# Kernel optimization log

Measured on AMD Instinct MI355X. Metric: run time of the kernel, lower is better.

The kernel has to match this reference:

```python
import jax, jax.numpy as jnp
import numpy as np

# ChebConv normalization (sym, lambda_max=2.0 default):
# L_hat = 2/lambda_max * (I - D^-1/2 A D^-1/2) - I = -D^-1/2 A D^-1/2 (plus 0/-1 diag for deg>0/deg==0)

def _norm(edge_weight, src, dst, N):
    deg = jax.ops.segment_sum(edge_weight, src, num_segments=N)
    d = jnp.where(deg > 0, deg ** -0.5, 0.0)
    norm = -d[src] * edge_weight * d[dst]          # off-diagonal entries of L_hat
    diag = d * d * deg - 1.0                        # 0 where deg>0, -1 where deg==0
    return norm, diag

def _prop(z, norm, diag, src, dst, N):
    # y = L_hat @ z, message passing source->target
    agg = jax.ops.segment_sum(norm[:, None] * z[src], dst, num_segments=N)
    return agg + diag[:, None] * z

def _cheb(h, theta, bias, norm, diag, src, dst, N):
    # theta: [K, H, H]; Chebyshev recurrence T_k = 2 L_hat T_{k-1} - T_{k-2}
    Tx0 = h
    out = Tx0 @ theta[0]
    Tx1 = _prop(Tx0, norm, diag, src, dst, N)
    out = out + Tx1 @ theta[1]
    for k in range(2, theta.shape[0]):
        Tx2 = 2.0 * _prop(Tx1, norm, diag, src, dst, N) - Tx0
        out = out + Tx2 @ theta[k]
        Tx0, Tx1 = Tx1, Tx2
    return out + bias

def setup_inputs() -> dict:
    N, E, F_IN, H, K = 50000, 1600000, 64, 64, 3
    key = jax.random.key(0)
    ks = jax.random.split(key, 12)
    s = 0.05
    x = jax.random.normal(ks[0], (N, F_IN), jnp.float32)
    edge_index = jax.random.randint(ks[1], (2, E), 0, N, jnp.int32)
    edge_weight = jax.random.uniform(ks[2], (E,), jnp.float32)
    h = jax.random.normal(ks[3], (N, H), jnp.float32)
    c = jax.random.normal(ks[4], (N, H), jnp.float32)
    W_x = jax.random.normal(ks[5], (4, F_IN, H), jnp.float32) * s   # W_i, W_f, W_c, W_o
    w_c = jax.random.normal(ks[6], (3, H), jnp.float32) * s          # w_c_i, w_c_f, w_c_o
    b = jax.random.normal(ks[7], (4, H), jnp.float32) * s            # b_i, b_f, b_c, b_o
    theta = jax.random.normal(ks[8], (4, K, H, H), jnp.float32) * s  # ChebConv weights per gate
    conv_b = jax.random.normal(ks[9], (4, H), jnp.float32) * s       # ChebConv biases per gate
    lin_w = jax.random.normal(ks[10], (H, H), jnp.float32) * s
    lin_b = jax.random.normal(ks[11], (H,), jnp.float32) * s
    return dict(x=x, edge_index=edge_index, edge_weight=edge_weight, h=h, c=c,
                W_x=W_x, w_c=w_c, b=b, theta=theta, conv_b=conv_b,
                lin_w=lin_w, lin_b=lin_b)

def reference(x, edge_index, edge_weight, h, c, W_x, w_c, b, theta, conv_b, lin_w, lin_b):
    N = x.shape[0]
    src, dst = edge_index[0], edge_index[1]
    norm, diag = _norm(edge_weight, src, dst, N)
    I = jax.nn.sigmoid(x @ W_x[0] + _cheb(h, theta[0], conv_b[0], norm, diag, src, dst, N) + w_c[0] * c + b[0])
    Fg = jax.nn.sigmoid(x @ W_x[1] + _cheb(h, theta[1], conv_b[1], norm, diag, src, dst, N) + w_c[1] * c + b[1])
    T = jnp.tanh(x @ W_x[2] + _cheb(h, theta[2], conv_b[2], norm, diag, src, dst, N) + b[2])
    Cn = Fg * c + I * T
    O = jax.nn.sigmoid(x @ W_x[3] + _cheb(h, theta[3], conv_b[3], norm, diag, src, dst, N) + w_c[2] * Cn + b[3])
    Hn = O * jnp.tanh(Cn)
    h_out = jax.nn.relu(Hn) @ lin_w + lin_b
    return (h_out, Hn, Cn)
```

## Files before the change

### kernel.cpp

```cpp
#include <hip/hip_runtime.h>
#include <math.h>


#define KCAP 80

__global__ void init_pack(float* __restrict__ deg, int* __restrict__ cnt,
                          const float* __restrict__ W_x, const float* __restrict__ theta,
                          float* __restrict__ Wbig, int N) {
    int idx = blockIdx.x * blockDim.x + threadIdx.x;
    if (idx < N) { deg[idx] = 0.f; cnt[idx] = 0; }
    if (idx < 4 * 64 * 256) {
        int s = idx >> 14;
        int rem = idx & 16383;
        int k = rem >> 8;
        int cj = rem & 255;
        int g = cj >> 6;
        int j = cj & 63;
        float v = (s == 0) ? W_x[((size_t)g * 64 + k) * 64 + j]
                           : theta[(((size_t)g * 3 + (s - 1)) * 64 + k) * 64 + j];
        Wbig[idx] = v;
    }
}

__global__ void edge_fused(const int* __restrict__ ei, const float* __restrict__ w,
                           float* __restrict__ deg, int* __restrict__ cnt,
                           int2* __restrict__ slots, int E) {
    int t = blockIdx.x * blockDim.x + threadIdx.x;
    int e = t * 4;
    if (e + 3 < E && (E & 3) == 0) {
        int4 s4 = *reinterpret_cast<const int4*>(ei + e);
        int4 d4 = *reinterpret_cast<const int4*>(ei + E + e);
        float4 w4 = *reinterpret_cast<const float4*>(w + e);
        atomicAdd(&deg[s4.x], w4.x);
        atomicAdd(&deg[s4.y], w4.y);
        atomicAdd(&deg[s4.z], w4.z);
        atomicAdd(&deg[s4.w], w4.w);
        int p0 = atomicAdd(&cnt[d4.x], 1);
        int p1 = atomicAdd(&cnt[d4.y], 1);
        int p2 = atomicAdd(&cnt[d4.z], 1);
        int p3 = atomicAdd(&cnt[d4.w], 1);
        if (p0 < KCAP) slots[(size_t)d4.x * KCAP + p0] = make_int2(s4.x, __float_as_int(w4.x));
        if (p1 < KCAP) slots[(size_t)d4.y * KCAP + p1] = make_int2(s4.y, __float_as_int(w4.y));
        if (p2 < KCAP) slots[(size_t)d4.z * KCAP + p2] = make_int2(s4.z, __float_as_int(w4.z));
        if (p3 < KCAP) slots[(size_t)d4.w * KCAP + p3] = make_int2(s4.w, __float_as_int(w4.w));
    } else {
        for (int q = e; q < e + 4 && q < E; ++q) {
            int s = ei[q];
            int d = ei[E + q];
            float wv = w[q];
            atomicAdd(&deg[s], wv);
            int p = atomicAdd(&cnt[d], 1);
            if (p < KCAP) slots[(size_t)d * KCAP + p] = make_int2(s, __float_as_int(wv));
        }
    }
}

__global__ __launch_bounds__(256)
void node_prep(const float* __restrict__ deg, const float* __restrict__ h,
               float* __restrict__ dinv, float* __restrict__ diagv,
               float* __restrict__ zs1, int N) {
    int idx = blockIdx.x * 256 + threadIdx.x;
    if (idx >= N * 64) return;
    int i = idx >> 6;
    float dg = deg[i];
    float dv = (dg > 0.f) ? 1.0f / sqrtf(dg) : 0.f;
    if ((idx & 63) == 0) {
        dinv[i] = dv;
        diagv[i] = (dg > 0.f) ? dv * dv * dg - 1.0f : -1.0f;
    }
    zs1[idx] = dv * h[idx];
}

__global__ __launch_bounds__(256)
void spmm_slots(const float* __restrict__ zfull, const float* __restrict__ zsc,
                const float* __restrict__ diagv, const float* __restrict__ dinv,
                const int* __restrict__ cnt, const int2* __restrict__ slots,
                const float* __restrict__ hsub, float alpha,
                float* __restrict__ out, float* __restrict__ zscOut, int N) {
    const int wq = __builtin_amdgcn_readfirstlane(threadIdx.x >> 6);
    const int r = blockIdx.x * 4 + wq;
    const int lane = threadIdx.x & 63;
    if (r >= N) return;
    const int n = min(cnt[r], KCAP);
    const float dgv = diagv[r];
    const float dvv = dinv[r];
    float g = 0.f;
    const int4* s4 = reinterpret_cast<const int4*>(slots + (size_t)r * KCAP);
    int p = 0;
    for (; p + 7 < n; p += 8) {
        const int q = p >> 1;
        int4 a = s4[q + 0];
        int4 b = s4[q + 1];
        int4 cc = s4[q + 2];
        int4 d = s4[q + 3];
        float z0 = zsc[(size_t)a.x * 64 + lane];
        float z1 = zsc[(size_t)a.z * 64 + lane];
        float z2 = zsc[(size_t)b.x * 64 + lane];
        float z3 = zsc[(size_t)b.z * 64 + lane];
        float z4 = zsc[(size_t)cc.x * 64 + lane];
        float z5 = zsc[(size_t)cc.z * 64 + lane];
        float z6 = zsc[(size_t)d.x * 64 + lane];
        float z7 = zsc[(size_t)d.z * 64 + lane];
        g += __int_as_float(a.y) * z0;
        g += __int_as_float(a.w) * z1;
        g += __int_as_float(b.y) * z2;
        g += __int_as_float(b.w) * z3;
        g += __int_as_float(cc.y) * z4;
        g += __int_as_float(cc.w) * z5;
        g += __int_as_float(d.y) * z6;
        g += __int_as_float(d.w) * z7;
    }
    const int2* s2 = slots + (size_t)r * KCAP;
    for (; p < n; ++p) {
        int2 eSlot = s2[p];
        g += __int_as_float(eSlot.y) * zsc[(size_t)eSlot.x * 64 + lane];
    }
    float val = dgv * zfull[(size_t)r * 64 + lane] - dvv * g;
    float res = alpha * val;
    if (hsub) res -= hsub[(size_t)r * 64 + lane];
    out[(size_t)r * 64 + lane] = res;
    if (zscOut) zscOut[(size_t)r * 64 + lane] = dvv * res;
}

__device__ __forceinline__ float sigf_(float v) { return 1.0f / (1.0f + __expf(-v)); }
__device__ __forceinline__ float tanhf_(float v) { return 2.0f / (1.0f + __expf(-2.0f * v)) - 1.0f; }

__global__ __launch_bounds__(256, 4)
void gemm_gates(const float* __restrict__ x, const float* __restrict__ h,
                const float* __restrict__ Tx1, const float* __restrict__ Tx2,
                const float* __restrict__ Wbig, const float* __restrict__ c,
                const float* __restrict__ w_c, const float* __restrict__ bb,
                const float* __restrict__ conv_b, const float* __restrict__ lin_w,
                const float* __restrict__ lin_b,
                float* __restrict__ out, int N) {
    __shared__ __align__(16) float At[32][64];
    __shared__ __align__(16) float Bs[8192];
    const int tid = threadIdx.x;
    const int tx = tid & 31;
    const int ty = tid >> 5;
    const int row0 = blockIdx.x * 64;

    float acc[8][8];
#pragma unroll
    for (int i = 0; i < 8; ++i)
#pragma unroll
        for (int j = 0; j < 8; ++j) acc[i][j] = 0.f;

    const float* Asrc[4] = {x, h, Tx1, Tx2};

    for (int s = 0; s < 4; ++s) {
        const float* A = Asrc[s];
#pragma unroll
        for (int hf = 0; hf < 2; ++hf) {
            __syncthreads();
            {
                const int mi = tid & 63;
                const int kc = tid >> 6;
                const int gr = row0 + mi;
#pragma unroll
                for (int rep = 0; rep < 2; ++rep) {
                    const int kl = rep * 16 + kc * 4;
                    float4 v = make_float4(0.f, 0.f, 0.f, 0.f);
                    if (gr < N) v = *reinterpret_cast<const float4*>(A + (size_t)gr * 64 + hf * 32 + kl);
                    At[kl + 0][mi] = v.x;
                    At[kl + 1][mi] = v.y;
                    At[kl + 2][mi] = v.z;
                    At[kl + 3][mi] = v.w;
                }
            }
            {
                const float4* B4 = reinterpret_cast<const float4*>(Wbig + ((size_t)s * 64 + hf * 32) * 256);
                float4* Bf4 = reinterpret_cast<float4*>(Bs);
#pragma unroll
                for (int rep = 0; rep < 8; ++rep) {
                    int i4 = rep * 256 + tid;
                    Bf4[i4] = B4[i4];
                }
            }
            __syncthreads();
#pragma unroll 4
            for (int k = 0; k < 32; ++k) {
                float av[8], bv[8];
                *reinterpret_cast<float4*>(av)     = *reinterpret_cast<const float4*>(&At[k][ty * 8]);
                *reinterpret_cast<float4*>(av + 4) = *reinterpret_cast<const float4*>(&At[k][ty * 8 + 4]);
                *reinterpret_cast<float4*>(bv)     = *reinterpret_cast<const float4*>(&Bs[k * 256 + tx * 4]);
                *reinterpret_cast<float4*>(bv + 4) = *reinterpret_cast<const float4*>(&Bs[k * 256 + 128 + tx * 4]);
#pragma unroll
                for (int i = 0; i < 8; ++i)
#pragma unroll
                    for (int j = 0; j < 8; ++j) acc[i][j] += av[i] * bv[j];
            }
        }
    }

    __syncthreads();

    const int jbase = (tx & 15) * 4;
    const bool loT = (tx < 16);
    const size_t No64 = (size_t)N * 64;

    const float4 cbI = *reinterpret_cast<const float4*>(conv_b + jbase);
    const float4 cbF = *reinterpret_cast<const float4*>(conv_b + 64 + jbase);
    const float4 cbT = *reinterpret_cast<const float4*>(conv_b + 128 + jbase);
    const float4 cbO = *reinterpret_cast<const float4*>(conv_b + 192 + jbase);
    const float4 bI  = *reinterpret_cast<const float4*>(bb + jbase);
    const float4 bF  = *reinterpret_cast<const float4*>(bb + 64 + jbase);
    const float4 bT  = *reinterpret_cast<const float4*>(bb + 128 + jbase);
    const float4 bO  = *reinterpret_cast<const float4*>(bb + 192 + jbase);
    const float4 wI  = *reinterpret_cast<const float4*>(w_c + jbase);
    const float4 wF  = *reinterpret_cast<const float4*>(w_c + 64 + jbase);
    const float4 wO  = *reinterpret_cast<const float4*>(w_c + 128 + jbase);

#pragma unroll
    for (int i = 0; i < 8; ++i) {
        const int li = ty * 8 + i;
        const int gi = row0 + li;
        float4 cv4 = make_float4(0.f, 0.f, 0.f, 0.f);
        if (gi < N) cv4 = *reinterpret_cast<const float4*>(c + (size_t)gi * 64 + jbase);
        float hn[4], cn[4];
#pragma unroll
        for (int jj = 0; jj < 4; ++jj) {
            float mine0 = acc[i][jj];
            float mine1 = acc[i][4 + jj];
            float oth0 = __shfl_xor(mine0, 16, 64);
            float oth1 = __shfl_xor(mine1, 16, 64);
            float pI = loT ? mine0 : oth0;
            float pF = loT ? oth0 : mine0;
            float pT = loT ? mine1 : oth1;
            float pO = loT ? oth1 : mine1;
            const float cv = (&cv4.x)[jj];
            pI += (&cbI.x)[jj] + (&bI.x)[jj] + (&wI.x)[jj] * cv;
            pF += (&cbF.x)[jj] + (&bF.x)[jj] + (&wF.x)[jj] * cv;
            pT += (&cbT.x)[jj] + (&bT.x)[jj];
            float Ig = sigf_(pI);
            float Fg = sigf_(pF);
            float Tg = tanhf_(pT);
            float Cn = Fg * cv + Ig * Tg;
            pO += (&cbO.x)[jj] + (&bO.x)[jj] + (&wO.x)[jj] * Cn;
            float Og = sigf_(pO);
            float Hn = Og * tanhf_(Cn);
            hn[jj] = Hn;
            cn[jj] = Cn;
            if (loT) {
                int j = jbase + jj;
                Bs[j * 64 + (((li & ~3) ^ (j & 28)) + (li & 3))] = fmaxf(Hn, 0.f);
            }
        }
        if (gi < N) {
            if (loT)
                *reinterpret_cast<float4*>(out + No64 + (size_t)gi * 64 + jbase) =
                    make_float4(hn[0], hn[1], hn[2], hn[3]);
            else
                *reinterpret_cast<float4*>(out + No64 * 2 + (size_t)gi * 64 + jbase) =
                    make_float4(cn[0], cn[1], cn[2], cn[3]);
        }
    }
    __syncthreads();

    {
        const int ri = tid >> 4;
        const int ci = tid & 15;
        float a2[4][4];
#pragma unroll
        for (int i = 0; i < 4; ++i)
#pragma unroll
            for (int j = 0; j < 4; ++j) a2[i][j] = 0.f;
#pragma unroll 4
        for (int k = 0; k < 64; ++k) {
            float4 av4 = *reinterpret_cast<const float4*>(&Bs[k * 64 + ((ri * 4) ^ (k & 28))]);
            float4 bv4 = *reinterpret_cast<const float4*>(lin_w + k * 64 + ci * 4);
            a2[0][0] += av4.x * bv4.x; a2[0][1] += av4.x * bv4.y; a2[0][2] += av4.x * bv4.z; a2[0][3] += av4.x * bv4.w;
            a2[1][0] += av4.y * bv4.x; a2[1][1] += av4.y * bv4.y; a2[1][2] += av4.y * bv4.z; a2[1][3] += av4.y * bv4.w;
            a2[2][0] += av4.z * bv4.x; a2[2][1] += av4.z * bv4.y; a2[2][2] += av4.z * bv4.z; a2[2][3] += av4.z * bv4.w;
            a2[3][0] += av4.w * bv4.x; a2[3][1] += av4.w * bv4.y; a2[3][2] += av4.w * bv4.z; a2[3][3] += av4.w * bv4.w;
        }
        float4 bias = *reinterpret_cast<const float4*>(lin_b + ci * 4);
#pragma unroll
        for (int i = 0; i < 4; ++i) {
            int gr = row0 + ri * 4 + i;
            if (gr < N) {
                float4 o = make_float4(a2[i][0] + bias.x, a2[i][1] + bias.y,
                                       a2[i][2] + bias.z, a2[i][3] + bias.w);
                *reinterpret_cast<float4*>(out + (size_t)gr * 64 + ci * 4) = o;
            }
        }
    }
}

extern "C" void kernel_launch(void* const* d_in, const int* in_sizes, int n_in,
                              void* d_out, int out_size, void* d_ws, size_t ws_size,
                              hipStream_t stream) {
    const float* x        = (const float*)d_in[0];
    const int* edge_index = (const int*)d_in[1];
    const float* edge_w   = (const float*)d_in[2];
    const float* h        = (const float*)d_in[3];
    const float* c        = (const float*)d_in[4];
    const float* W_x      = (const float*)d_in[5];
    const float* w_c      = (const float*)d_in[6];
    const float* b        = (const float*)d_in[7];
    const float* theta    = (const float*)d_in[8];
    const float* conv_b   = (const float*)d_in[9];
    const float* lin_w    = (const float*)d_in[10];
    const float* lin_b    = (const float*)d_in[11];
    float* out = (float*)d_out;

    const int N = in_sizes[0] / 64;
    const int E = in_sizes[2];

    char* wsb = (char*)d_ws;
    size_t off = 0;
    auto carve = [&](size_t bytes) -> void* {
        void* p = wsb + off;
        off = (off + bytes + 255) & ~(size_t)255;
        return p;
    };
    float* deg   = (float*)carve((size_t)N * 4);
    int*   cnt   = (int*)  carve((size_t)N * 4);
    float* dinv  = (float*)carve((size_t)N * 4);
    float* diagv = (float*)carve((size_t)N * 4);
    int2*  slots = (int2*) carve((size_t)N * KCAP * 8);
    float* Tx1   = (float*)carve((size_t)N * 64 * 4);
    float* Tx2   = (float*)carve((size_t)N * 64 * 4);
    float* zsT   = (float*)carve((size_t)N * 64 * 4);
    float* Wbig  = (float*)carve((size_t)4 * 64 * 256 * 4);
    float* zs1   = Tx2;

    const int initElems = (N > 65536) ? N : 65536;
    init_pack<<<(initElems + 255) / 256, 256, 0, stream>>>(deg, cnt, W_x, theta, Wbig, N);
    edge_fused<<<((E + 3) / 4 + 255) / 256, 256, 0, stream>>>(edge_index, edge_w, deg, cnt, slots, E);
    node_prep<<<((N * 64) + 255) / 256, 256, 0, stream>>>(deg, h, dinv, diagv, zs1, N);
    spmm_slots<<<(N + 3) / 4, 256, 0, stream>>>(h, zs1, diagv, dinv, cnt, slots,
                                                nullptr, 1.0f, Tx1, zsT, N);
    spmm_slots<<<(N + 3) / 4, 256, 0, stream>>>(Tx1, zsT, diagv, dinv, cnt, slots,
                                                h, 2.0f, Tx2, nullptr, N);
    gemm_gates<<<(N + 63) / 64, 256, 0, stream>>>(x, h, Tx1, Tx2, Wbig, c, w_c, b, conv_b,
                                                  lin_w, lin_b, out, N);
}
```

Measured before the change: 525.5 us.

## Overlap x/h gate GEMM with edge scatter and drop pre-scaled z buffers

Fuses the edge atomic scatter with the x and h slices of the gate GEMM into one launch whose blocks interleave, so the compute-bound GEMM hides latency behind the atomic-bound edge pass. The partial products go to a new N×256 PRE buffer that the final gate kernel loads as its starting accumulator, so it only multiplies Tx1 and Tx2. It also removes the pre-scaled zs buffers: node_prep only computes dinv and diag, and the SpMM multiplies by dinv[src] per neighbor. This costs an extra scalar gather per edge and extra PRE read/write traffic, and it depends on the workspace being large enough.

```diff
diff --git a/kernel.cpp b/kernel.cpp
--- a/kernel.cpp
+++ b/kernel.cpp
@@ -22,61 +22,138 @@
     }
 }
 
-__global__ void edge_fused(const int* __restrict__ ei, const float* __restrict__ w,
-                           float* __restrict__ deg, int* __restrict__ cnt,
-                           int2* __restrict__ slots, int E) {
-    int t = blockIdx.x * blockDim.x + threadIdx.x;
-    int e = t * 4;
-    if (e + 3 < E && (E & 3) == 0) {
-        int4 s4 = *reinterpret_cast<const int4*>(ei + e);
-        int4 d4 = *reinterpret_cast<const int4*>(ei + E + e);
-        float4 w4 = *reinterpret_cast<const float4*>(w + e);
-        atomicAdd(&deg[s4.x], w4.x);
-        atomicAdd(&deg[s4.y], w4.y);
-        atomicAdd(&deg[s4.z], w4.z);
-        atomicAdd(&deg[s4.w], w4.w);
-        int p0 = atomicAdd(&cnt[d4.x], 1);
-        int p1 = atomicAdd(&cnt[d4.y], 1);
-        int p2 = atomicAdd(&cnt[d4.z], 1);
-        int p3 = atomicAdd(&cnt[d4.w], 1);
-        if (p0 < KCAP) slots[(size_t)d4.x * KCAP + p0] = make_int2(s4.x, __float_as_int(w4.x));
-        if (p1 < KCAP) slots[(size_t)d4.y * KCAP + p1] = make_int2(s4.y, __float_as_int(w4.y));
-        if (p2 < KCAP) slots[(size_t)d4.z * KCAP + p2] = make_int2(s4.z, __float_as_int(w4.z));
-        if (p3 < KCAP) slots[(size_t)d4.w * KCAP + p3] = make_int2(s4.w, __float_as_int(w4.w));
-    } else {
-        for (int q = e; q < e + 4 && q < E; ++q) {
-            int s = ei[q];
-            int d = ei[E + q];
-            float wv = w[q];
-            atomicAdd(&deg[s], wv);
-            int p = atomicAdd(&cnt[d], 1);
-            if (p < KCAP) slots[(size_t)d * KCAP + p] = make_int2(s, __float_as_int(wv));
+__global__ __launch_bounds__(256, 4)
+void edge_gemmxh(const int* __restrict__ ei, const float* __restrict__ w,
+                 float* __restrict__ deg, int* __restrict__ cnt,
+                 int2* __restrict__ slots, int E, int EB,
+                 const float* __restrict__ x, const float* __restrict__ h,
+                 const float* __restrict__ Wbig, float* __restrict__ PRE,
+                 int N, int GB) {
+    __shared__ __align__(16) float At[32][64];
+    __shared__ __align__(16) float Bs[8192];
+    const int bi = blockIdx.x;
+    bool isGemm;
+    int sub;
+    if (GB > 0 && bi < 2 * GB) { isGemm = (bi & 1); sub = bi >> 1; }
+    else { isGemm = false; sub = GB + (bi - 2 * GB); }
+
+    if (!isGemm) {
+        if (sub >= EB) return;
+        const int e = (sub * 256 + threadIdx.x) * 4;
+        if (e + 3 < E && (E & 3) == 0) {
+            int4 s4 = *reinterpret_cast<const int4*>(ei + e);
+            int4 d4 = *reinterpret_cast<const int4*>(ei + E + e);
+            float4 w4 = *reinterpret_cast<const float4*>(w + e);
+            atomicAdd(&deg[s4.x], w4.x);
+            atomicAdd(&deg[s4.y], w4.y);
+            atomicAdd(&deg[s4.z], w4.z);
+            atomicAdd(&deg[s4.w], w4.w);
+            int p0 = atomicAdd(&cnt[d4.x], 1);
+            int p1 = atomicAdd(&cnt[d4.y], 1);
+            int p2 = atomicAdd(&cnt[d4.z], 1);
+            int p3 = atomicAdd(&cnt[d4.w], 1);
+            if (p0 < KCAP) slots[(size_t)d4.x * KCAP + p0] = make_int2(s4.x, __float_as_int(w4.x));
+            if (p1 < KCAP) slots[(size_t)d4.y * KCAP + p1] = make_int2(s4.y, __float_as_int(w4.y));
+            if (p2 < KCAP) slots[(size_t)d4.z * KCAP + p2] = make_int2(s4.z, __float_as_int(w4.z));
+            if (p3 < KCAP) slots[(size_t)d4.w * KCAP + p3] = make_int2(s4.w, __float_as_int(w4.w));
+        } else {
+            for (int q = e; q < e + 4 && q < E; ++q) {
+                int s = ei[q];
+                int d = ei[E + q];
+                float wv = w[q];
+                atomicAdd(&deg[s], wv);
+                int p = atomicAdd(&cnt[d], 1);
+                if (p < KCAP) slots[(size_t)d * KCAP + p] = make_int2(s, __float_as_int(wv));
+            }
+        }
+        return;
+    }
+
+    const int tid = threadIdx.x;
+    const int tx = tid & 31;
+    const int ty = tid >> 5;
+    const int row0 = sub * 64;
+
+    float acc[8][8];
+#pragma unroll
+    for (int i = 0; i < 8; ++i)
+#pragma unroll
+        for (int j = 0; j < 8; ++j) acc[i][j] = 0.f;
+
+    const float* Asrc[2] = {x, h};
+    for (int s = 0; s < 2; ++s) {
+        const float* A = Asrc[s];
+#pragma unroll
+        for (int hf = 0; hf < 2; ++hf) {
+            __syncthreads();
+            {
+                const int mi = tid & 63;
+                const int kc = tid >> 6;
+                const int gr = row0 + mi;
+#pragma unroll
+                for (int rep = 0; rep < 2; ++rep) {
+                    const int kl = rep * 16 + kc * 4;
+                    float4 v = make_float4(0.f, 0.f, 0.f, 0.f);
+                    if (gr < N) v = *reinterpret_cast<const float4*>(A + (size_t)gr * 64 + hf * 32 + kl);
+                    At[kl + 0][mi] = v.x;
+                    At[kl + 1][mi] = v.y;
+                    At[kl + 2][mi] = v.z;
+                    At[kl + 3][mi] = v.w;
+                }
+            }
+            {
+                const float4* B4 = reinterpret_cast<const float4*>(Wbig + ((size_t)s * 64 + hf * 32) * 256);
+                float4* Bf4 = reinterpret_cast<float4*>(Bs);
+#pragma unroll
+                for (int rep = 0; rep < 8; ++rep) {
+                    int i4 = rep * 256 + tid;
+                    Bf4[i4] = B4[i4];
+                }
+            }
+            __syncthreads();
+#pragma unroll 4
+            for (int k = 0; k < 32; ++k) {
+                float av[8], bv[8];
+                *reinterpret_cast<float4*>(av)     = *reinterpret_cast<const float4*>(&At[k][ty * 8]);
+                *reinterpret_cast<float4*>(av + 4) = *reinterpret_cast<const float4*>(&At[k][ty * 8 + 4]);
+                *reinterpret_cast<float4*>(bv)     = *reinterpret_cast<const float4*>(&Bs[k * 256 + tx * 4]);
+                *reinterpret_cast<float4*>(bv + 4) = *reinterpret_cast<const float4*>(&Bs[k * 256 + 128 + tx * 4]);
+#pragma unroll
+                for (int i = 0; i < 8; ++i)
+#pragma unroll
+                    for (int j = 0; j < 8; ++j) acc[i][j] += av[i] * bv[j];
+            }
+        }
+    }
+#pragma unroll
+    for (int i = 0; i < 8; ++i) {
+        const int gi = row0 + ty * 8 + i;
+        if (gi < N) {
+            *reinterpret_cast<float4*>(PRE + (size_t)gi * 256 + tx * 4) =
+                make_float4(acc[i][0], acc[i][1], acc[i][2], acc[i][3]);
+            *reinterpret_cast<float4*>(PRE + (size_t)gi * 256 + 128 + tx * 4) =
+                make_float4(acc[i][4], acc[i][5], acc[i][6], acc[i][7]);
         }
     }
 }
 
 __global__ __launch_bounds__(256)
-void node_prep(const float* __restrict__ deg, const float* __restrict__ h,
-               float* __restrict__ dinv, float* __restrict__ diagv,
-               float* __restrict__ zs1, int N) {
-    int idx = blockIdx.x * 256 + threadIdx.x;
-    if (idx >= N * 64) return;
-    int i = idx >> 6;
-    float dg = deg[i];
-    float dv = (dg > 0.f) ? 1.0f / sqrtf(dg) : 0.f;
-    if ((idx & 63) == 0) {
+void node_prep(const float* __restrict__ deg, float* __restrict__ dinv,
+               float* __restrict__ diagv, int N) {
+    int i = blockIdx.x * 256 + threadIdx.x;
+    if (i < N) {
+        float dg = deg[i];
+        float dv = (dg > 0.f) ? 1.0f / sqrtf(dg) : 0.f;
         dinv[i] = dv;
         diagv[i] = (dg > 0.f) ? dv * dv * dg - 1.0f : -1.0f;
     }
-    zs1[idx] = dv * h[idx];
 }
 
 __global__ __launch_bounds__(256)
-void spmm_slots(const float* __restrict__ zfull, const float* __restrict__ zsc,
-                const float* __restrict__ diagv, const float* __restrict__ dinv,
-                const int* __restrict__ cnt, const int2* __restrict__ slots,
-                const float* __restrict__ hsub, float alpha,
-                float* __restrict__ out, float* __restrict__ zscOut, int N) {
+void spmm_slots(const float* __restrict__ z, const float* __restrict__ diagv,
+                const float* __restrict__ dinv, const int* __restrict__ cnt,
+                const int2* __restrict__ slots, const float* __restrict__ hsub,
+                float alpha, float* __restrict__ out, int N) {
     const int wq = __builtin_amdgcn_readfirstlane(threadIdx.x >> 6);
     const int r = blockIdx.x * 4 + wq;
     const int lane = threadIdx.x & 63;
@@ -93,33 +170,33 @@
         int4 b = s4[q + 1];
         int4 cc = s4[q + 2];
         int4 d = s4[q + 3];
-        float z0 = zsc[(size_t)a.x * 64 + lane];
-        float z1 = zsc[(size_t)a.z * 64 + lane];
-        float z2 = zsc[(size_t)b.x * 64 + lane];
-        float z3 = zsc[(size_t)b.z * 64 + lane];
-        float z4 = zsc[(size_t)cc.x * 64 + lane];
-        float z5 = zsc[(size_t)cc.z * 64 + lane];
-        float z6 = zsc[(size_t)d.x * 64 + lane];
-        float z7 = zsc[(size_t)d.z * 64 + lane];
-        g += __int_as_float(a.y) * z0;
-        g += __int_as_float(a.w) * z1;
-        g += __int_as_float(b.y) * z2;
-        g += __int_as_float(b.w) * z3;
-        g += __int_as_float(cc.y) * z4;
-        g += __int_as_float(cc.w) * z5;
-        g += __int_as_float(d.y) * z6;
-        g += __int_as_float(d.w) * z7;
+        float d0 = dinv[a.x], d1 = dinv[a.z], d2 = dinv[b.x], d3 = dinv[b.z];
+        float d4v = dinv[cc.x], d5 = dinv[cc.z], d6 = dinv[d.x], d7 = dinv[d.z];
+        float z0 = z[(size_t)a.x * 64 + lane];
+        float z1 = z[(size_t)a.z * 64 + lane];
+        float z2 = z[(size_t)b.x * 64 + lane];
+        float z3 = z[(size_t)b.z * 64 + lane];
+        float z4 = z[(size_t)cc.x * 64 + lane];
+        float z5 = z[(size_t)cc.z * 64 + lane];
+        float z6 = z[(size_t)d.x * 64 + lane];
+        float z7 = z[(size_t)d.z * 64 + lane];
+        g += __int_as_float(a.y) * (d0 * z0);
+        g += __int_as_float(a.w) * (d1 * z1);
+        g += __int_as_float(b.y) * (d2 * z2);
+        g += __int_as_float(b.w) * (d3 * z3);
+        g += __int_as_float(cc.y) * (d4v * z4);
+        g += __int_as_float(cc.w) * (d5 * z5);
+        g += __int_as_float(d.y) * (d6 * z6);
+        g += __int_as_float(d.w) * (d7 * z7);
     }
     const int2* s2 = slots + (size_t)r * KCAP;
     for (; p < n; ++p) {
         int2 eSlot = s2[p];
-        g += __int_as_float(eSlot.y) * zsc[(size_t)eSlot.x * 64 + lane];
-    }
-    float val = dgv * zfull[(size_t)r * 64 + lane] - dvv * g;
-    float res = alpha * val;
+        g += __int_as_float(eSlot.y) * (dinv[eSlot.x] * z[(size_t)eSlot.x * 64 + lane]);
+    }
+    float res = alpha * (dgv * z[(size_t)r * 64 + lane] - dvv * g);
     if (hsub) res -= hsub[(size_t)r * 64 + lane];
     out[(size_t)r * 64 + lane] = res;
-    if (zscOut) zscOut[(size_t)r * 64 + lane] = dvv * res;
 }
 
 __device__ __forceinline__ float sigf_(float v) { return 1.0f / (1.0f + __expf(-v)); }
@@ -128,7 +205,8 @@
 __global__ __launch_bounds__(256, 4)
 void gemm_gates(const float* __restrict__ x, const float* __restrict__ h,
                 const float* __restrict__ Tx1, const float* __restrict__ Tx2,
-                const float* __restrict__ Wbig, const float* __restrict__ c,
+                const float* __restrict__ Wbig, const float* __restrict__ PRE,
+                const float* __restrict__ c,
                 const float* __restrict__ w_c, const float* __restrict__ bb,
                 const float* __restrict__ conv_b, const float* __restrict__ lin_w,
                 const float* __restrict__ lin_b,
@@ -141,14 +219,30 @@
     const int row0 = blockIdx.x * 64;
 
     float acc[8][8];
-#pragma unroll
-    for (int i = 0; i < 8; ++i)
-#pragma unroll
-        for (int j = 0; j < 8; ++j) acc[i][j] = 0.f;
+    if (PRE) {
+#pragma unroll
+        for (int i = 0; i < 8; ++i) {
+            const int gi = row0 + ty * 8 + i;
+            float4 lo = make_float4(0.f, 0.f, 0.f, 0.f);
+            float4 hi = make_float4(0.f, 0.f, 0.f, 0.f);
+            if (gi < N) {
+                lo = *reinterpret_cast<const float4*>(PRE + (size_t)gi * 256 + tx * 4);
+                hi = *reinterpret_cast<const float4*>(PRE + (size_t)gi * 256 + 128 + tx * 4);
+            }
+            acc[i][0] = lo.x; acc[i][1] = lo.y; acc[i][2] = lo.z; acc[i][3] = lo.w;
+            acc[i][4] = hi.x; acc[i][5] = hi.y; acc[i][6] = hi.z; acc[i][7] = hi.w;
+        }
+    } else {
+#pragma unroll
+        for (int i = 0; i < 8; ++i)
+#pragma unroll
+            for (int j = 0; j < 8; ++j) acc[i][j] = 0.f;
+    }
 
     const float* Asrc[4] = {x, h, Tx1, Tx2};
-
-    for (int s = 0; s < 4; ++s) {
+    const int s0 = PRE ? 2 : 0;
+
+    for (int s = s0; s < 4; ++s) {
         const float* A = Asrc[s];
 #pragma unroll
         for (int hf = 0; hf < 2; ++hf) {
@@ -306,6 +400,8 @@
 
     const int N = in_sizes[0] / 64;
     const int E = in_sizes[2];
+    const int EB = (E + 1023) / 1024;
+    const int GB = (N + 63) / 64;
 
     char* wsb = (char*)d_ws;
     size_t off = 0;
@@ -321,18 +417,24 @@
     int2*  slots = (int2*) carve((size_t)N * KCAP * 8);
     float* Tx1   = (float*)carve((size_t)N * 64 * 4);
     float* Tx2   = (float*)carve((size_t)N * 64 * 4);
-    float* zsT   = (float*)carve((size_t)N * 64 * 4);
     float* Wbig  = (float*)carve((size_t)4 * 64 * 256 * 4);
-    float* zs1   = Tx2;
+    float* PRE   = (float*)carve((size_t)N * 256 * 4);
+    const bool usePre = (off <= ws_size);
 
     const int initElems = (N > 65536) ? N : 65536;
     init_pack<<<(initElems + 255) / 256, 256, 0, stream>>>(deg, cnt, W_x, theta, Wbig, N);
-    edge_fused<<<((E + 3) / 4 + 255) / 256, 256, 0, stream>>>(edge_index, edge_w, deg, cnt, slots, E);
-    node_prep<<<((N * 64) + 255) / 256, 256, 0, stream>>>(deg, h, dinv, diagv, zs1, N);
-    spmm_slots<<<(N + 3) / 4, 256, 0, stream>>>(h, zs1, diagv, dinv, cnt, slots,
-                                                nullptr, 1.0f, Tx1, zsT, N);
-    spmm_slots<<<(N + 3) / 4, 256, 0, stream>>>(Tx1, zsT, diagv, dinv, cnt, slots,
-                                                h, 2.0f, Tx2, nullptr, N);
-    gemm_gates<<<(N + 63) / 64, 256, 0, stream>>>(x, h, Tx1, Tx2, Wbig, c, w_c, b, conv_b,
-                                                  lin_w, lin_b, out, N);
-}
+    if (usePre) {
+        edge_gemmxh<<<EB + GB, 256, 0, stream>>>(edge_index, edge_w, deg, cnt, slots, E, EB,
+                                                 x, h, Wbig, PRE, N, GB);
+    } else {
+        edge_gemmxh<<<EB, 256, 0, stream>>>(edge_index, edge_w, deg, cnt, slots, E, EB,
+                                            x, h, Wbig, nullptr, N, 0);
+    }
+    node_prep<<<(N + 255) / 256, 256, 0, stream>>>(deg, dinv, diagv, N);
+    spmm_slots<<<(N + 3) / 4, 256, 0, stream>>>(h, diagv, dinv, cnt, slots,
+                                                nullptr, 1.0f, Tx1, N);
+    spmm_slots<<<(N + 3) / 4, 256, 0, stream>>>(Tx1, diagv, dinv, cnt, slots,
+                                                h, 2.0f, Tx2, N);
+    gemm_gates<<<GB, 256, 0, stream>>>(x, h, Tx1, Tx2, Wbig, usePre ? PRE : nullptr,
+                                       c, w_c, b, conv_b, lin_w, lin_b, out, N);
+}
```

After: 476.4 us. -9.3%, faster.
